# Kernel tuning notes

Measured on AMD Instinct MI355X. Metric: run time of the kernel, lower is better.

The kernel has to match this reference:

```python
import jax, jax.numpy as jnp
import numpy as np

V, L, H, D = 2048, 16, 8, 64   # vocab, max_chars, n_head, word_vec_d
B = 8192                        # number of words in batch (rows of char_code)
NW_TOTAL = 8192                 # len(word_code)
N_NAMES = 2048                  # total names (4 words each)
N_GROUPS = 8                    # groups of names (256 each)
PAD = 0
TEMP = D ** 0.5
LN_EPS = 1e-5


def make_pos():
    freq = D // 2
    inv = 1.0 / np.power(10000.0, np.arange(freq) / freq)
    ph = np.outer(np.arange(L), inv)
    return jnp.asarray(np.hstack([np.cos(ph), np.sin(ph)]).astype(np.float32))


def setup_inputs() -> dict:
    key = jax.random.key(0)
    ks = jax.random.split(key, 8)
    char_emb = jax.random.normal(ks[0], (V, D), jnp.float32) * 0.02
    char_emb = char_emb.at[PAD].set(0.0)  # padding_idx row
    Wc = jax.random.normal(ks[1], (D, 3 * H * D), jnp.float32) * 0.02
    bc = jnp.zeros((3 * H * D,), jnp.float32)
    Wp = jax.random.normal(ks[2], (D, 3 * H * D), jnp.float32) * 0.02
    bp = jnp.zeros((3 * H * D,), jnp.float32)
    gamma = jnp.ones((D,), jnp.float32)
    beta = jnp.zeros((D,), jnp.float32)
    W1 = jax.random.normal(ks[3], (H, 16), jnp.float32) * 0.1
    b1 = jnp.zeros((16,), jnp.float32)
    W2 = jax.random.normal(ks[4], (16, 8), jnp.float32) * 0.1
    b2 = jnp.zeros((8,), jnp.float32)
    char_code = jax.random.randint(ks[5], (B, L), 1, V)
    char_code = char_code.at[::4, -2:].set(PAD)  # some padded tails
    word_code = jax.random.randint(ks[6], (NW_TOTAL,), 0, B)
    n_words = np.full((N_NAMES,), NW_TOTAL // N_NAMES, dtype=np.int64)
    n_names = np.full((N_GROUPS,), N_NAMES // N_GROUPS, dtype=np.int64)
    return {"char_emb": char_emb, "Wc": Wc, "bc": bc, "Wp": Wp, "bp": bp,
            "gamma": gamma, "beta": beta, "W1": W1, "b1": b1, "W2": W2, "b2": b2,
            "char_code": char_code, "word_code": word_code,
            "n_words": n_words, "n_names": n_names}


def reference(char_emb, Wc, bc, Wp, bp, gamma, beta, W1, b1, W2, b2,
              char_code, word_code, n_words, n_names):
    pos = make_pos()
    # ComputeQKV: linear d -> 3*H*d, reshape [N,3,H,D]
    cqkv = (char_emb @ Wc + bc).reshape(V, 3, H, D)
    cq, ck, cv = cqkv[:, 0], cqkv[:, 1], cqkv[:, 2]        # [V,H,D]
    pqkv = (pos @ Wp + bp).reshape(L, 3, H, D)
    pq, pk, pv = pqkv[:, 0], pqkv[:, 1], pqkv[:, 2]        # [L,H,D]
    # precomputed score tables
    char_qk = jnp.einsum('xhd,yhd->hxy', cq, ck).at[:, :, PAD].set(-1e9)  # [H,V,V]
    pos_qk = jnp.einsum('xhd,yhd->hxy', pq, pk)                            # [H,L,L]
    # char_q@pos_k + (pos_q@char_k)^T summed over the first dim of char_pos_qk
    cp = jnp.einsum('vhd,lhd->hvl', cq, pk) + jnp.einsum('lhd,vhd->hvl', pq, ck)  # [H,V,L]
    code = char_code                                        # [B,L]
    # gather-assembled scores, no [H,B*L,V] intermediate
    sim = (char_qk[:, code[:, :, None], code[:, None, :]]   # [H,B,L,L]
           + cp[:, code]
           + pos_qk[:, None]) / TEMP
    attn = jax.nn.softmax(sim, axis=-1)                     # [H,B,L,L] (dropout=0)
    v = jnp.transpose(cv[code], (2, 0, 1, 3)) + pv.transpose(1, 0, 2)[:, None]  # [H,B,L,D]
    out = jnp.einsum('hbij,hbjd->bihd', attn, v)            # [B,L,H,D]
    mu = out.mean(-1, keepdims=True)
    var = out.var(-1, keepdims=True)
    out = (out - mu) / jnp.sqrt(var + LN_EPS) * gamma + beta  # LayerNorm(D)
    char_ft = jnp.transpose(out, (0, 2, 1, 3))              # [B,H,L,D]
    mask = (code != PAD)
    pooled = jnp.einsum('bl,bhld->bhd', mask.astype(out.dtype), char_ft) \
             / mask.sum(-1)[:, None, None]                  # masked mean over chars
    x = jnp.transpose(pooled, (0, 2, 1))                    # [B,D,H]
    x = jax.nn.relu(x @ W1 + b1) @ W2 + b2                  # MLP over head dim -> [B,D,8]
    word_ft = x.reshape(B, -1)[word_code]                   # [NW_TOTAL, D*8]
    nw = np.asarray(n_words)
    seg = jnp.asarray(np.repeat(np.arange(nw.size), nw))
    name_ft = jax.ops.segment_sum(word_ft, seg, num_segments=nw.size) \
              / jnp.asarray(nw, word_ft.dtype)[:, None]     # ragged mean -> [N_NAMES, D*8]
    splits = np.cumsum(np.asarray(n_names))[:-1]
    return tuple(jnp.split(name_ft, splits, axis=0))
```

## Files before the change

kernel.cpp:

```cpp
#include <hip/hip_runtime.h>
#include <hip/hip_bf16.h>
#include <math.h>

typedef __attribute__((ext_vector_type(8))) short bfrag;
typedef __attribute__((ext_vector_type(4))) float ffrag;
typedef __attribute__((ext_vector_type(4))) float f4v;
typedef __attribute__((ext_vector_type(2))) float f2v;

#define C3 1536
#define PS 24

__device__ __forceinline__ unsigned short f2bf(float f) {
    unsigned u = __float_as_uint(f);
    return (unsigned short)((u + 0x7FFFu + ((u >> 16) & 1u)) >> 16);
}

__device__ __forceinline__ float row16_sum(float x) {
    int v;
    v = __builtin_amdgcn_update_dpp(0, __float_as_int(x), 0xB1, 0xF, 0xF, true);
    x += __int_as_float(v);
    v = __builtin_amdgcn_update_dpp(0, __float_as_int(x), 0x4E, 0xF, 0xF, true);
    x += __int_as_float(v);
    v = __builtin_amdgcn_update_dpp(0, __float_as_int(x), 0x124, 0xF, 0xF, true);
    x += __int_as_float(v);
    v = __builtin_amdgcn_update_dpp(0, __float_as_int(x), 0x128, 0xF, 0xF, true);
    x += __int_as_float(v);
    return x;
}

__global__ __launch_bounds__(256) void precompute_kernel(
    const float* __restrict__ char_emb, const float* __restrict__ Wc, const float* __restrict__ bc,
    const float* __restrict__ Wp, const float* __restrict__ bp,
    const float* __restrict__ gamma, const float* __restrict__ beta,
    unsigned short* __restrict__ cqkv, unsigned short* __restrict__ pbf,
    unsigned short* __restrict__ pvb, float* __restrict__ gbtab)
{
    const int b = blockIdx.x;
    const int t = threadIdx.x;
    if (b < 1536) {
        const int mt = b / 6;
        const int nt = b - mt * 6;
        const int m0 = mt * 8;
        const int c = nt * 256 + t;
        const float qs = (c < 512) ? 0.125f : 1.f;
        const float bias = bc[c];
        float acc[8];
        #pragma unroll
        for (int r = 0; r < 8; ++r) acc[r] = bias;
        #pragma unroll 16
        for (int dd = 0; dd < 64; ++dd) {
            const float wv = Wc[dd * C3 + c];
            #pragma unroll
            for (int r = 0; r < 8; ++r)
                acc[r] = fmaf(char_emb[(m0 + r) * 64 + dd], wv, acc[r]);
        }
        #pragma unroll
        for (int r = 0; r < 8; ++r)
            cqkv[(size_t)(m0 + r) * C3 + c] = f2bf(acc[r] * qs);
    } else {
        const int e = b - 1536;
        const int l = e / 6;
        const int cc = e - l * 6;
        if (b == 1536 && t < 64) {
            #pragma unroll
            for (int dt = 0; dt < 4; ++dt) {
                gbtab[t * 8 + dt]     = gamma[dt * 16 + t];
                gbtab[t * 8 + 4 + dt] = beta[dt * 16 + t];
            }
        }
        __shared__ float spos[64];
        if (t < 64) {
            const int f = t & 31;
            const float inv = exp2f(-(float)f * 0.41524101186092034f);
            const float ph = (float)l * inv;
            spos[t] = (t < 32) ? cosf(ph) : sinf(ph);
        }
        __syncthreads();
        const int c = t + cc * 256;
        float acc = bp[c];
        #pragma unroll
        for (int dd = 0; dd < 64; ++dd)
            acc = fmaf(spos[dd], Wp[dd * C3 + c], acc);
        if (c < 1024) {
            const float qs = (c < 512) ? 0.125f : 1.f;
            pbf[(c >> 6) * 1024 + l * 64 + (c & 63)] = f2bf(acc * qs);
        } else {
            const int h = (c >> 6) & 7, d = c & 63;
            pvb[((h * 4 + (d >> 4)) * 2 + (l >> 3)) * 128 + (d & 15) * 8 + (l & 7)] = f2bf(acc);
        }
    }
}

__global__ __launch_bounds__(256, 4) void attn_kernel(
    const unsigned short* __restrict__ cqkv, const unsigned short* __restrict__ pbf,
    const unsigned short* __restrict__ pvb, const int* __restrict__ char_code,
    const float* __restrict__ gbtab,
    const float* __restrict__ W1, const float* __restrict__ b1,
    const float* __restrict__ W2, const float* __restrict__ b2,
    float* __restrict__ x)
{
    __shared__ __attribute__((aligned(16))) unsigned short sVt[8 * 1024];
    __shared__ __attribute__((aligned(16))) unsigned short sP[8 * 16 * PS];
    __shared__ float sPool[512];
    __shared__ float sHid[64 * 17];
    __shared__ float sWb[280];

    const int t = threadIdx.x;
    const int lane = t & 63;
    const int wid = t >> 6;
    const int w = blockIdx.x;
    const int quad = lane >> 4;
    const int n = lane & 15;
    const int q2 = quad & 1;

    if (t < 128) { sWb[t] = W1[t]; sWb[144 + t] = W2[t]; }
    else if (t < 144) sWb[t] = b1[t - 128];
    else if (t < 152) sWb[272 + (t - 144)] = b2[t - 144];

    const int code = char_code[w * 16 + n];
    const bool kvalid = (code != 0);
    const unsigned long long msk = __ballot(kvalid);
    const int nv = __popcll(msk & 0xFFFFull);

    const f4v g4 = *(const f4v*)(gbtab + n * 8);
    const f4v b4 = *(const f4v*)(gbtab + n * 8 + 4);

    #pragma unroll
    for (int c2 = 0; c2 < 2; ++c2) {
        const int h = wid + c2 * 4;
        unsigned short* vt = sVt + h * 1024;
        const unsigned short* cvp = cqkv + (size_t)code * C3 + 1024 + h * 64;
        #pragma unroll
        for (int cc = 0; cc < 2; ++cc) {
            const int d8 = quad + cc * 4;
            const bfrag cv = *(const bfrag*)(cvp + d8 * 8);
            #pragma unroll
            for (int j = 0; j < 8; ++j) {
                const int d = d8 * 8 + j;
                const int e = ((d >> 4) * 2 + (n >> 3)) * 128
                            + ((d & 15) ^ ((n >> 3) << 2)) * 8 + (n & 7);
                vt[e] = (unsigned short)cv[j];
            }
        }
    }

    ffrag accS[2];
    #pragma unroll
    for (int c2 = 0; c2 < 2; ++c2) { ffrag z = {0.f,0.f,0.f,0.f}; accS[c2] = z; }
    #pragma unroll
    for (int c2 = 0; c2 < 2; ++c2) {
        const int h = wid + c2 * 4;
        const unsigned short* cbase = cqkv + (size_t)code * C3 + h * 64;
        const unsigned short* pq = pbf + h * 1024 + n * 64;
        const unsigned short* pk = pbf + (8 + h) * 1024 + n * 64;
        #pragma unroll
        for (int cc = 0; cc < 2; ++cc) {
            const int off = quad * 8 + cc * 32;
            const bfrag cqF = *(const bfrag*)(cbase + off);
            const bfrag ckF = *(const bfrag*)(cbase + 512 + off);
            const bfrag pqF = *(const bfrag*)(pq + off);
            const bfrag pkF = *(const bfrag*)(pk + off);
            accS[c2] = __builtin_amdgcn_mfma_f32_16x16x32_bf16(cqF, ckF, accS[c2], 0, 0, 0);
            accS[c2] = __builtin_amdgcn_mfma_f32_16x16x32_bf16(cqF, pkF, accS[c2], 0, 0, 0);
            accS[c2] = __builtin_amdgcn_mfma_f32_16x16x32_bf16(ckF, pqF, accS[c2], 0, 0, 0);
            accS[c2] = __builtin_amdgcn_mfma_f32_16x16x32_bf16(pqF, pkF, accS[c2], 0, 0, 0);
        }
    }

    #pragma unroll
    for (int c2 = 0; c2 < 2; ++c2) {
        const int h = wid + c2 * 4;
        unsigned short* pt = sP + h * 16 * PS;
        #pragma unroll
        for (int r = 0; r < 4; ++r) {
            const float pr = kvalid ? __expf(accS[c2][r]) : 0.f;
            pt[(quad * 4 + r) * PS + n] = f2bf(pr);
        }
    }

    bfrag onesf;
    #pragma unroll
    for (int j = 0; j < 8; ++j) onesf[j] = (short)0x3F80;

    #pragma unroll
    for (int c2 = 0; c2 < 2; ++c2) {
        const int h = wid + c2 * 4;
        unsigned short* pt = sP + h * 16 * PS;
        unsigned short* vt = sVt + h * 1024;
        bfrag ap;
        #pragma unroll
        for (int j = 0; j < 8; ++j) ap[j] = 0;
        if (quad < 2) ap = *(const bfrag*)(pt + n * PS + quad * 8);
        ffrag accO[4];
        #pragma unroll
        for (int dt = 0; dt < 4; ++dt) { ffrag z = {0.f,0.f,0.f,0.f}; accO[dt] = z; }
        #pragma unroll
        for (int dt = 0; dt < 4; ++dt) {
            const bfrag bcv = *(const bfrag*)(vt + (dt * 2 + q2) * 128 + (n ^ (q2 << 2)) * 8);
            accO[dt] = __builtin_amdgcn_mfma_f32_16x16x32_bf16(ap, bcv, accO[dt], 0, 0, 0);
            const bfrag bpv = *(const bfrag*)(pvb + ((h * 4 + dt) * 2 + q2) * 128 + n * 8);
            accO[dt] = __builtin_amdgcn_mfma_f32_16x16x32_bf16(ap, bpv, accO[dt], 0, 0, 0);
        }
        ffrag accE = {0.f, 0.f, 0.f, 0.f};
        accE = __builtin_amdgcn_mfma_f32_16x16x32_bf16(ap, onesf, accE, 0, 0, 0);

        float ps1[4], ps2[4];
        #pragma unroll
        for (int r = 0; r < 4; ++r) {
            ps1[r] = accO[0][r] + accO[1][r] + accO[2][r] + accO[3][r];
            ps2[r] = accO[0][r]*accO[0][r] + accO[1][r]*accO[1][r]
                   + accO[2][r]*accO[2][r] + accO[3][r]*accO[3][r];
            ps1[r] = row16_sum(ps1[r]);
            ps2[r] = row16_sum(ps2[r]);
        }
        float pool[4] = {0.f, 0.f, 0.f, 0.f};
        #pragma unroll
        for (int r = 0; r < 4; ++r) {
            const float mu   = ps1[r] * 0.015625f;
            const float var  = fmaxf(ps2[r] * 0.015625f - mu * mu, 0.f);
            const float rstd = rsqrtf(var + accE[r] * accE[r] * 1e-5f);
            const float iv = ((msk >> (quad * 4 + r)) & 1ull) ? 1.f : 0.f;
            #pragma unroll
            for (int dt = 0; dt < 4; ++dt)
                pool[dt] += iv * fmaf((accO[dt][r] - mu) * rstd, g4[dt], b4[dt]);
        }
        #pragma unroll
        for (int xm = 16; xm <= 32; xm <<= 1) {
            #pragma unroll
            for (int dt = 0; dt < 4; ++dt) pool[dt] += __shfl_xor(pool[dt], xm);
        }
        if (quad == 0) {
            const float invnv = 1.f / (float)nv;
            #pragma unroll
            for (int dt = 0; dt < 4; ++dt)
                sPool[h * 64 + n * 4 + dt] = pool[dt] * invnv;
        }
    }
    __syncthreads();

    if (t < 64) {
        const int dmap = (t & 15) * 4 + (t >> 4);
        float pl[8];
        #pragma unroll
        for (int hh = 0; hh < 8; ++hh) pl[hh] = sPool[hh * 64 + dmap];
        #pragma unroll
        for (int c = 0; c < 16; ++c) {
            float hs = sWb[128 + c];
            #pragma unroll
            for (int hh = 0; hh < 8; ++hh) hs = fmaf(pl[hh], sWb[hh * 16 + c], hs);
            sHid[t * 17 + c] = fmaxf(hs, 0.f);
        }
    }
    __syncthreads();
    {
        const int d = t >> 2, o0 = (t & 3) * 2;
        float a0 = sWb[272 + o0], a1 = sWb[272 + o0 + 1];
        #pragma unroll
        for (int c = 0; c < 16; ++c) {
            const float hc = sHid[d * 17 + c];
            a0 = fmaf(hc, sWb[144 + c * 8 + o0], a0);
            a1 = fmaf(hc, sWb[144 + c * 8 + o0 + 1], a1);
        }
        f2v res; res[0] = a0; res[1] = a1;
        *(f2v*)(x + (size_t)w * 512 + t * 2) = res;
    }
}

__global__ __launch_bounds__(256) void name_avg_kernel(
    const float* __restrict__ x, const int* __restrict__ word_code,
    const int* __restrict__ n_words, float* __restrict__ out)
{
    const int t = threadIdx.x;
    const int lane = t & 63;
    const int nm = blockIdx.x * 4 + (t >> 6);

    int part = 0;
    for (int i = lane; i < nm; i += 64) part += n_words[i];
    #pragma unroll
    for (int xm = 1; xm <= 32; xm <<= 1) part += __shfl_xor(part, xm);
    const int off = part;
    const int cnt = n_words[nm];

    f4v a0 = {0.f,0.f,0.f,0.f}, a1 = {0.f,0.f,0.f,0.f};
    for (int r = 0; r < cnt; ++r) {
        const int wc = word_code[off + r];
        const f4v u0 = *(const f4v*)(x + (size_t)wc * 512 + lane * 8);
        const f4v u1 = *(const f4v*)(x + (size_t)wc * 512 + lane * 8 + 4);
        #pragma unroll
        for (int k = 0; k < 4; ++k) { a0[k] += u0[k]; a1[k] += u1[k]; }
    }
    const float inv = 1.f / (float)cnt;
    #pragma unroll
    for (int k = 0; k < 4; ++k) { a0[k] *= inv; a1[k] *= inv; }
    *(f4v*)(out + (size_t)nm * 512 + lane * 8) = a0;
    *(f4v*)(out + (size_t)nm * 512 + lane * 8 + 4) = a1;
}

extern "C" void kernel_launch(void* const* d_in, const int* in_sizes, int n_in,
                              void* d_out, int out_size, void* d_ws, size_t ws_size,
                              hipStream_t stream) {
    (void)in_sizes; (void)n_in; (void)out_size; (void)ws_size;
    const float* char_emb = (const float*)d_in[0];
    const float* Wc    = (const float*)d_in[1];
    const float* bc    = (const float*)d_in[2];
    const float* Wp    = (const float*)d_in[3];
    const float* bp    = (const float*)d_in[4];
    const float* gamma = (const float*)d_in[5];
    const float* beta  = (const float*)d_in[6];
    const float* W1    = (const float*)d_in[7];
    const float* b1    = (const float*)d_in[8];
    const float* W2    = (const float*)d_in[9];
    const float* b2    = (const float*)d_in[10];
    const int* char_code = (const int*)d_in[11];
    const int* word_code = (const int*)d_in[12];
    const int* n_words   = (const int*)d_in[13];

    char* ws = (char*)d_ws;
    unsigned short* cqkv = (unsigned short*)ws;
    unsigned short* pbf  = (unsigned short*)(ws + 6291456);
    unsigned short* pvb  = (unsigned short*)(ws + 6324224);
    float* x     = (float*)(ws + 6340608);
    float* gbtab = (float*)(ws + 23117824);
    float* out = (float*)d_out;

    precompute_kernel<<<1632, 256, 0, stream>>>(char_emb, Wc, bc, Wp, bp, gamma, beta,
                                                cqkv, pbf, pvb, gbtab);
    attn_kernel<<<8192, 256, 0, stream>>>(cqkv, pbf, pvb, char_code, gbtab,
                                          W1, b1, W2, b2, x);
    name_avg_kernel<<<512, 256, 0, stream>>>(x, word_code, n_words, out);
}
```

Measured before the change: 200.5 us.

## Stage per-word QK rows in LDS with coalesced loads, one wave per head

The attention kernel now uses 512 threads, one wave per head, instead of four waves each handling two heads. It loads each character's Q/K rows into shared memory with coalesced 16-byte loads instead of per-lane scattered gathers. The positional Q/K table is re-laid out in precompute so the MFMA fragments are read contiguously by lane. The aim is less gather inefficiency and more parallelism per block. The cost is a larger shared-memory footprint (about 56KB with aliasing) and an extra barrier, which may lower occupancy.

```diff
diff --git a/kernel.cpp b/kernel.cpp
--- a/kernel.cpp
+++ b/kernel.cpp
@@ -5,10 +5,10 @@
 typedef __attribute__((ext_vector_type(8))) short bfrag;
 typedef __attribute__((ext_vector_type(4))) float ffrag;
 typedef __attribute__((ext_vector_type(4))) float f4v;
-typedef __attribute__((ext_vector_type(2))) float f2v;
 
 #define C3 1536
 #define PS 24
+#define QKS 1032
 
 __device__ __forceinline__ unsigned short f2bf(float f) {
     unsigned u = __float_as_uint(f);
@@ -32,7 +32,7 @@
     const float* __restrict__ char_emb, const float* __restrict__ Wc, const float* __restrict__ bc,
     const float* __restrict__ Wp, const float* __restrict__ bp,
     const float* __restrict__ gamma, const float* __restrict__ beta,
-    unsigned short* __restrict__ cqkv, unsigned short* __restrict__ pbf,
+    unsigned short* __restrict__ cqkv, unsigned short* __restrict__ pqf,
     unsigned short* __restrict__ pvb, float* __restrict__ gbtab)
 {
     const int b = blockIdx.x;
@@ -83,7 +83,9 @@
             acc = fmaf(spos[dd], Wp[dd * C3 + c], acc);
         if (c < 1024) {
             const float qs = (c < 512) ? 0.125f : 1.f;
-            pbf[(c >> 6) * 1024 + l * 64 + (c & 63)] = f2bf(acc * qs);
+            const int s = c >> 9, h = (c >> 6) & 7, d = c & 63;
+            pqf[s * 8192 + ((h * 2 + (d >> 5)) * 64 + ((d >> 3) & 3) * 16 + l) * 8 + (d & 7)]
+                = f2bf(acc * qs);
         } else {
             const int h = (c >> 6) & 7, d = c & 63;
             pvb[((h * 4 + (d >> 4)) * 2 + (l >> 3)) * 128 + (d & 15) * 8 + (l & 7)] = f2bf(acc);
@@ -91,23 +93,25 @@
     }
 }
 
-__global__ __launch_bounds__(256, 4) void attn_kernel(
-    const unsigned short* __restrict__ cqkv, const unsigned short* __restrict__ pbf,
+__global__ __launch_bounds__(512, 4) void attn_kernel(
+    const unsigned short* __restrict__ cqkv, const unsigned short* __restrict__ pqf,
     const unsigned short* __restrict__ pvb, const int* __restrict__ char_code,
     const float* __restrict__ gbtab,
     const float* __restrict__ W1, const float* __restrict__ b1,
     const float* __restrict__ W2, const float* __restrict__ b2,
     float* __restrict__ x)
 {
-    __shared__ __attribute__((aligned(16))) unsigned short sVt[8 * 1024];
-    __shared__ __attribute__((aligned(16))) unsigned short sP[8 * 16 * PS];
-    __shared__ float sPool[512];
-    __shared__ float sHid[64 * 17];
+    __shared__ __attribute__((aligned(16))) unsigned char sBuf[55552];
     __shared__ float sWb[280];
+    unsigned short* sQK = (unsigned short*)sBuf;
+    unsigned short* sVt = (unsigned short*)(sBuf + 33024);
+    unsigned short* sP  = (unsigned short*)(sBuf + 49408);
+    float* sPool = (float*)sBuf;
+    float* sHid  = (float*)(sBuf + 2048);
 
     const int t = threadIdx.x;
     const int lane = t & 63;
-    const int wid = t >> 6;
+    const int h = t >> 6;
     const int w = blockIdx.x;
     const int quad = lane >> 4;
     const int n = lane & 15;
@@ -126,115 +130,103 @@
     const f4v b4 = *(const f4v*)(gbtab + n * 8 + 4);
 
     #pragma unroll
-    for (int c2 = 0; c2 < 2; ++c2) {
-        const int h = wid + c2 * 4;
-        unsigned short* vt = sVt + h * 1024;
-        const unsigned short* cvp = cqkv + (size_t)code * C3 + 1024 + h * 64;
-        #pragma unroll
-        for (int cc = 0; cc < 2; ++cc) {
-            const int d8 = quad + cc * 4;
-            const bfrag cv = *(const bfrag*)(cvp + d8 * 8);
-            #pragma unroll
-            for (int j = 0; j < 8; ++j) {
-                const int d = d8 * 8 + j;
-                const int e = ((d >> 4) * 2 + (n >> 3)) * 128
-                            + ((d & 15) ^ ((n >> 3) << 2)) * 8 + (n & 7);
-                vt[e] = (unsigned short)cv[j];
-            }
-        }
-    }
-
-    ffrag accS[2];
-    #pragma unroll
-    for (int c2 = 0; c2 < 2; ++c2) { ffrag z = {0.f,0.f,0.f,0.f}; accS[c2] = z; }
-    #pragma unroll
-    for (int c2 = 0; c2 < 2; ++c2) {
-        const int h = wid + c2 * 4;
-        const unsigned short* cbase = cqkv + (size_t)code * C3 + h * 64;
-        const unsigned short* pq = pbf + h * 1024 + n * 64;
-        const unsigned short* pk = pbf + (8 + h) * 1024 + n * 64;
+    for (int r = 0; r < 2; ++r) {
+        const int row = h + r * 8;
+        const int rcode = __shfl(code, row);
+        const unsigned short* base = cqkv + (size_t)rcode * C3;
+        #pragma unroll
+        for (int c = 0; c < 2; ++c)
+            *(bfrag*)(sQK + row * QKS + c * 512 + lane * 8)
+                = *(const bfrag*)(base + c * 512 + lane * 8);
+        const bfrag vv = *(const bfrag*)(base + 1024 + lane * 8);
+        const int vh = lane >> 3, d0 = (lane & 7) * 8;
+        #pragma unroll
+        for (int j = 0; j < 8; ++j) {
+            const int d = d0 + j;
+            const int e = vh * 1024 + ((d >> 4) * 2 + (row >> 3)) * 128
+                        + ((d & 15) ^ ((row >> 3) << 2)) * 8 + (row & 7);
+            sVt[e] = (unsigned short)vv[j];
+        }
+    }
+    __syncthreads();
+
+    ffrag accS = {0.f, 0.f, 0.f, 0.f};
+    {
+        const unsigned short* qrow = sQK + n * QKS + h * 64;
         #pragma unroll
         for (int cc = 0; cc < 2; ++cc) {
             const int off = quad * 8 + cc * 32;
-            const bfrag cqF = *(const bfrag*)(cbase + off);
-            const bfrag ckF = *(const bfrag*)(cbase + 512 + off);
-            const bfrag pqF = *(const bfrag*)(pq + off);
-            const bfrag pkF = *(const bfrag*)(pk + off);
-            accS[c2] = __builtin_amdgcn_mfma_f32_16x16x32_bf16(cqF, ckF, accS[c2], 0, 0, 0);
-            accS[c2] = __builtin_amdgcn_mfma_f32_16x16x32_bf16(cqF, pkF, accS[c2], 0, 0, 0);
-            accS[c2] = __builtin_amdgcn_mfma_f32_16x16x32_bf16(ckF, pqF, accS[c2], 0, 0, 0);
-            accS[c2] = __builtin_amdgcn_mfma_f32_16x16x32_bf16(pqF, pkF, accS[c2], 0, 0, 0);
-        }
-    }
-
-    #pragma unroll
-    for (int c2 = 0; c2 < 2; ++c2) {
-        const int h = wid + c2 * 4;
-        unsigned short* pt = sP + h * 16 * PS;
-        #pragma unroll
-        for (int r = 0; r < 4; ++r) {
-            const float pr = kvalid ? __expf(accS[c2][r]) : 0.f;
-            pt[(quad * 4 + r) * PS + n] = f2bf(pr);
-        }
-    }
-
+            const bfrag cqF = *(const bfrag*)(qrow + off);
+            const bfrag ckF = *(const bfrag*)(qrow + 512 + off);
+            const bfrag pqF = *(const bfrag*)(pqf + ((h * 2 + cc) * 64 + lane) * 8);
+            const bfrag pkF = *(const bfrag*)(pqf + 8192 + ((h * 2 + cc) * 64 + lane) * 8);
+            accS = __builtin_amdgcn_mfma_f32_16x16x32_bf16(cqF, ckF, accS, 0, 0, 0);
+            accS = __builtin_amdgcn_mfma_f32_16x16x32_bf16(cqF, pkF, accS, 0, 0, 0);
+            accS = __builtin_amdgcn_mfma_f32_16x16x32_bf16(ckF, pqF, accS, 0, 0, 0);
+            accS = __builtin_amdgcn_mfma_f32_16x16x32_bf16(pqF, pkF, accS, 0, 0, 0);
+        }
+    }
+
+    unsigned short* pt = sP + h * 16 * PS;
+    #pragma unroll
+    for (int r = 0; r < 4; ++r) {
+        const float pr = kvalid ? __expf(accS[r]) : 0.f;
+        pt[(quad * 4 + r) * PS + n] = f2bf(pr);
+    }
+
+    bfrag ap;
+    #pragma unroll
+    for (int j = 0; j < 8; ++j) ap[j] = 0;
+    if (quad < 2) ap = *(const bfrag*)(pt + n * PS + quad * 8);
+    unsigned short* vt = sVt + h * 1024;
+    ffrag accO[4];
+    #pragma unroll
+    for (int dt = 0; dt < 4; ++dt) { ffrag z = {0.f,0.f,0.f,0.f}; accO[dt] = z; }
+    #pragma unroll
+    for (int dt = 0; dt < 4; ++dt) {
+        const bfrag bcv = *(const bfrag*)(vt + (dt * 2 + q2) * 128 + (n ^ (q2 << 2)) * 8);
+        accO[dt] = __builtin_amdgcn_mfma_f32_16x16x32_bf16(ap, bcv, accO[dt], 0, 0, 0);
+        const bfrag bpv = *(const bfrag*)(pvb + ((h * 4 + dt) * 2 + q2) * 128 + n * 8);
+        accO[dt] = __builtin_amdgcn_mfma_f32_16x16x32_bf16(ap, bpv, accO[dt], 0, 0, 0);
+    }
     bfrag onesf;
     #pragma unroll
     for (int j = 0; j < 8; ++j) onesf[j] = (short)0x3F80;
-
-    #pragma unroll
-    for (int c2 = 0; c2 < 2; ++c2) {
-        const int h = wid + c2 * 4;
-        unsigned short* pt = sP + h * 16 * PS;
-        unsigned short* vt = sVt + h * 1024;
-        bfrag ap;
-        #pragma unroll
-        for (int j = 0; j < 8; ++j) ap[j] = 0;
-        if (quad < 2) ap = *(const bfrag*)(pt + n * PS + quad * 8);
-        ffrag accO[4];
-        #pragma unroll
-        for (int dt = 0; dt < 4; ++dt) { ffrag z = {0.f,0.f,0.f,0.f}; accO[dt] = z; }
-        #pragma unroll
-        for (int dt = 0; dt < 4; ++dt) {
-            const bfrag bcv = *(const bfrag*)(vt + (dt * 2 + q2) * 128 + (n ^ (q2 << 2)) * 8);
-            accO[dt] = __builtin_amdgcn_mfma_f32_16x16x32_bf16(ap, bcv, accO[dt], 0, 0, 0);
-            const bfrag bpv = *(const bfrag*)(pvb + ((h * 4 + dt) * 2 + q2) * 128 + n * 8);
-            accO[dt] = __builtin_amdgcn_mfma_f32_16x16x32_bf16(ap, bpv, accO[dt], 0, 0, 0);
-        }
-        ffrag accE = {0.f, 0.f, 0.f, 0.f};
-        accE = __builtin_amdgcn_mfma_f32_16x16x32_bf16(ap, onesf, accE, 0, 0, 0);
-
-        float ps1[4], ps2[4];
-        #pragma unroll
-        for (int r = 0; r < 4; ++r) {
-            ps1[r] = accO[0][r] + accO[1][r] + accO[2][r] + accO[3][r];
-            ps2[r] = accO[0][r]*accO[0][r] + accO[1][r]*accO[1][r]
-                   + accO[2][r]*accO[2][r] + accO[3][r]*accO[3][r];
-            ps1[r] = row16_sum(ps1[r]);
-            ps2[r] = row16_sum(ps2[r]);
-        }
-        float pool[4] = {0.f, 0.f, 0.f, 0.f};
-        #pragma unroll
-        for (int r = 0; r < 4; ++r) {
-            const float mu   = ps1[r] * 0.015625f;
-            const float var  = fmaxf(ps2[r] * 0.015625f - mu * mu, 0.f);
-            const float rstd = rsqrtf(var + accE[r] * accE[r] * 1e-5f);
-            const float iv = ((msk >> (quad * 4 + r)) & 1ull) ? 1.f : 0.f;
-            #pragma unroll
-            for (int dt = 0; dt < 4; ++dt)
-                pool[dt] += iv * fmaf((accO[dt][r] - mu) * rstd, g4[dt], b4[dt]);
-        }
-        #pragma unroll
-        for (int xm = 16; xm <= 32; xm <<= 1) {
-            #pragma unroll
-            for (int dt = 0; dt < 4; ++dt) pool[dt] += __shfl_xor(pool[dt], xm);
-        }
-        if (quad == 0) {
-            const float invnv = 1.f / (float)nv;
-            #pragma unroll
-            for (int dt = 0; dt < 4; ++dt)
-                sPool[h * 64 + n * 4 + dt] = pool[dt] * invnv;
-        }
+    ffrag accE = {0.f, 0.f, 0.f, 0.f};
+    accE = __builtin_amdgcn_mfma_f32_16x16x32_bf16(ap, onesf, accE, 0, 0, 0);
+
+    float ps1[4], ps2[4];
+    #pragma unroll
+    for (int r = 0; r < 4; ++r) {
+        ps1[r] = accO[0][r] + accO[1][r] + accO[2][r] + accO[3][r];
+        ps2[r] = accO[0][r]*accO[0][r] + accO[1][r]*accO[1][r]
+               + accO[2][r]*accO[2][r] + accO[3][r]*accO[3][r];
+        ps1[r] = row16_sum(ps1[r]);
+        ps2[r] = row16_sum(ps2[r]);
+    }
+    float pool[4] = {0.f, 0.f, 0.f, 0.f};
+    #pragma unroll
+    for (int r = 0; r < 4; ++r) {
+        const float mu   = ps1[r] * 0.015625f;
+        const float var  = fmaxf(ps2[r] * 0.015625f - mu * mu, 0.f);
+        const float rstd = rsqrtf(var + accE[r] * accE[r] * 1e-5f);
+        const float iv = ((msk >> (quad * 4 + r)) & 1ull) ? 1.f : 0.f;
+        #pragma unroll
+        for (int dt = 0; dt < 4; ++dt)
+            pool[dt] += iv * fmaf((accO[dt][r] - mu) * rstd, g4[dt], b4[dt]);
+    }
+    #pragma unroll
+    for (int xm = 16; xm <= 32; xm <<= 1) {
+        #pragma unroll
+        for (int dt = 0; dt < 4; ++dt) pool[dt] += __shfl_xor(pool[dt], xm);
+    }
+    const float invnv = 1.f / (float)nv;
+
+    __syncthreads();
+    if (quad == 0) {
+        #pragma unroll
+        for (int dt = 0; dt < 4; ++dt)
+            sPool[h * 64 + n * 4 + dt] = pool[dt] * invnv;
     }
     __syncthreads();
 
@@ -253,16 +245,12 @@
     }
     __syncthreads();
     {
-        const int d = t >> 2, o0 = (t & 3) * 2;
-        float a0 = sWb[272 + o0], a1 = sWb[272 + o0 + 1];
-        #pragma unroll
-        for (int c = 0; c < 16; ++c) {
-            const float hc = sHid[d * 17 + c];
-            a0 = fmaf(hc, sWb[144 + c * 8 + o0], a0);
-            a1 = fmaf(hc, sWb[144 + c * 8 + o0 + 1], a1);
-        }
-        f2v res; res[0] = a0; res[1] = a1;
-        *(f2v*)(x + (size_t)w * 512 + t * 2) = res;
+        const int d = t >> 3, o = t & 7;
+        float a = sWb[272 + o];
+        #pragma unroll
+        for (int c = 0; c < 16; ++c)
+            a = fmaf(sHid[d * 17 + c], sWb[144 + c * 8 + o], a);
+        x[(size_t)w * 512 + t] = a;
     }
 }
 
@@ -317,15 +305,15 @@
 
     char* ws = (char*)d_ws;
     unsigned short* cqkv = (unsigned short*)ws;
-    unsigned short* pbf  = (unsigned short*)(ws + 6291456);
+    unsigned short* pqf  = (unsigned short*)(ws + 6291456);
     unsigned short* pvb  = (unsigned short*)(ws + 6324224);
     float* x     = (float*)(ws + 6340608);
     float* gbtab = (float*)(ws + 23117824);
     float* out = (float*)d_out;
 
     precompute_kernel<<<1632, 256, 0, stream>>>(char_emb, Wc, bc, Wp, bp, gamma, beta,
-                                                cqkv, pbf, pvb, gbtab);
-    attn_kernel<<<8192, 256, 0, stream>>>(cqkv, pbf, pvb, char_code, gbtab,
+                                                cqkv, pqf, pvb, gbtab);
+    attn_kernel<<<8192, 512, 0, stream>>>(cqkv, pqf, pvb, char_code, gbtab,
                                           W1, b1, W2, b2, x);
     name_avg_kernel<<<512, 256, 0, stream>>>(x, word_code, n_words, out);
 }
```

Result: slower. 280.7 us (+40.0%).
